# Performance work log

Hardware: AMD Instinct MI355X
Metric: run time of the kernel (lower is better)

The kernel has to match this reference:

```python
import jax, jax.numpy as jnp
import numpy as np
from jax import lax

NTIME = 2048
NCOMP = 8
HID = 64
OUT = 64
MAX_EVENTS = NTIME * NCOMP
EVENT_DIM = NCOMP + 3


def setup_inputs() -> dict:
    key = jax.random.key(0)
    ks = jax.random.split(key, 10)
    B = 64
    s = lambda fan_in: 1.0 / np.sqrt(fan_in)
    return {
        "x": jax.random.uniform(ks[0], (B, NTIME, NCOMP), dtype=jnp.float32),
        "W1": jax.random.normal(ks[1], (EVENT_DIM, HID), dtype=jnp.float32) * s(EVENT_DIM),
        "b1": jax.random.normal(ks[2], (HID,), dtype=jnp.float32) * 0.01,
        "W2": jax.random.normal(ks[3], (HID, HID), dtype=jnp.float32) * s(HID),
        "b2": jax.random.normal(ks[4], (HID,), dtype=jnp.float32) * 0.01,
        "P1": jax.random.normal(ks[5], (HID + 1, HID), dtype=jnp.float32) * s(HID + 1),
        "pb1": jax.random.normal(ks[6], (HID,), dtype=jnp.float32) * 0.01,
        "P2": jax.random.normal(ks[7], (HID, OUT), dtype=jnp.float32) * s(HID),
        "pb2": jax.random.normal(ks[8], (OUT,), dtype=jnp.float32) * 0.01,
    }


def _event_table(x):
    # x: [B, T, C] float. Vectorized run-length encoding.
    B, T, C = x.shape
    seq = jnp.transpose((x > 0.5).astype(x.dtype), (0, 2, 1))  # [B, C, T] in {0,1}
    prev = jnp.concatenate([jnp.full((B, C, 1), -1.0, x.dtype), seq[:, :, :-1]], axis=-1)
    is_start = seq != prev  # t=0 always a start; [B, C, T] bool
    t_idx = jnp.arange(T, dtype=jnp.int32)
    # position of next run start strictly after t (T if none)
    start_pos = jnp.where(is_start, t_idx, T)  # [B, C, T] int32
    shifted = jnp.concatenate([start_pos[:, :, 1:], jnp.full((B, C, 1), T, jnp.int32)], axis=-1)
    next_start = lax.cummin(shifted, axis=2, reverse=True)  # suffix min
    dur = (next_start - t_idx).astype(x.dtype)  # run length at each start slot
    max_start = max(1, T - 1)
    start_norm = (t_idx.astype(x.dtype) / max_start)  # [T]
    onehot = jnp.broadcast_to(jnp.eye(C, dtype=x.dtype)[None, :, None, :], (B, C, T, C))
    feats = jnp.stack(
        [seq, jnp.broadcast_to(start_norm, (B, C, T)), dur / T], axis=-1
    )  # [B, C, T, 3]
    rows = jnp.concatenate([onehot, feats], axis=-1)  # [B, C, T, C+3]
    mask = is_start
    rows = rows * mask[..., None].astype(x.dtype)  # masked rows zero, as in torch
    return rows.reshape(B, C * T, C + 3), mask.reshape(B, C * T)


def reference(x, W1, b1, W2, b2, P1, pb1, P2, pb2):
    rows, mask = _event_table(x)  # [B, E, 11], [B, E]
    h = jax.nn.relu(rows @ W1 + b1) @ W2 + b2  # [B, E, HID]
    h = h * mask[..., None].astype(h.dtype)
    valid = jnp.maximum(mask.sum(axis=1, keepdims=True), 1).astype(h.dtype)  # [B, 1]
    pooled = h.sum(axis=1) / valid  # [B, HID]
    z = jnp.concatenate([pooled, valid / MAX_EVENTS], axis=-1)  # [B, HID+1]
    return jax.nn.relu(z @ P1 + pb1) @ P2 + pb2  # [B, OUT]
```

## Files before the change

kernel.cpp:

```cpp
#include <hip/hip_runtime.h>
#include <hip/hip_bf16.h>

#define T_LEN 2048
#define NCOMP 8
#define HID 64
#define OUT_DIM 64
#define BATCH 64
#define MAX_EVENTS (T_LEN * NCOMP)
#define NCHUNK 32
#define PART_STRIDE 66
#define NWAVE 8

typedef unsigned long long u64;

#define PARTIAL_BYTES (64ULL * NCOMP * PART_STRIDE * 4)

__global__ __launch_bounds__(512) void event_kernel(
    const float* __restrict__ x,
    const float* __restrict__ W1,
    const float* __restrict__ b1,
    float* __restrict__ partial)
{
    const int b    = blockIdx.x & 63;
    const int c    = blockIdx.x >> 6;
    const int tid  = threadIdx.x;
    const int lane = tid & 63;
    const int wave = tid >> 6;

    __shared__ u64 wsh[NCHUNK];
    __shared__ u64 tsh[NCHUNK];
    __shared__ int nxtf[NCHUNK + 1];
    __shared__ int wtot[NWAVE];
    __shared__ float4 elist[T_LEN];
    __shared__ float Sp[NWAVE][HID];

    const float4* xp = (const float4*)(x + ((size_t)b * T_LEN) * NCOMP);
    #pragma unroll
    for (int i = 0; i < 4; ++i) {
        int t = i * 512 + tid;
        float4 v0 = xp[t * 2];
        float4 v1 = xp[t * 2 + 1];
        unsigned m = 0;
        m |= (v0.x > 0.5f) ? 1u   : 0u;
        m |= (v0.y > 0.5f) ? 2u   : 0u;
        m |= (v0.z > 0.5f) ? 4u   : 0u;
        m |= (v0.w > 0.5f) ? 8u   : 0u;
        m |= (v1.x > 0.5f) ? 16u  : 0u;
        m |= (v1.y > 0.5f) ? 32u  : 0u;
        m |= (v1.z > 0.5f) ? 64u  : 0u;
        m |= (v1.w > 0.5f) ? 128u : 0u;
        u64 wd = __ballot((m >> c) & 1u);
        if (lane == 0) wsh[i * 8 + wave] = wd;
    }
    __syncthreads();

    if (tid < NCHUNK) {
        u64 w = wsh[tid];
        u64 carry = (tid > 0) ? (wsh[tid - 1] >> 63) : 0ULL;
        u64 tr = w ^ ((w << 1) | carry);
        if (tid == 0) tr |= 1ULL;
        tsh[tid] = tr;
        int first = tr ? tid * 64 + (__ffsll((long long)tr) - 1) : T_LEN;
        #pragma unroll
        for (int off = 1; off < NCHUNK; off <<= 1) {
            int v = __shfl_down(first, off);
            if (tid + off < NCHUNK) first = (v < first) ? v : first;
        }
        nxtf[tid] = first;
        if (tid == 0) nxtf[NCHUNK] = T_LEN;
    }
    __syncthreads();

    const int ch = tid >> 4;
    const int sh = (tid & 15) * 4;
    const u64 full  = tsh[ch];
    const u64 wbits = wsh[ch];
    unsigned tr4 = (unsigned)((full >> sh) & 0xFu);
    int nt = __popc(tr4);

    int incl = nt;
    #pragma unroll
    for (int o = 1; o < 64; o <<= 1) {
        int v = __shfl_up(incl, o);
        if (lane >= o) incl += v;
    }
    if (lane == 63) wtot[wave] = incl;
    __syncthreads();
    int waveoff = 0;
    for (int w = 0; w < wave; ++w) waveoff += wtot[w];
    int nE = 0;
    #pragma unroll
    for (int w = 0; w < NWAVE; ++w) nE += wtot[w];
    int off = waveoff + incl - nt;

    unsigned rem = tr4;
    while (rem) {
        int p = __ffs(rem) - 1;
        rem &= rem - 1;
        int t = (tid << 2) + p;
        unsigned s = (unsigned)((wbits >> (sh + p)) & 1ULL);
        int nxt;
        if (rem) {
            nxt = (tid << 2) + __ffs(rem) - 1;
        } else {
            int bp = sh + 4;
            u64 above = (bp >= 64) ? 0ULL : (full & (~0ULL << bp));
            nxt = above ? ch * 64 + (__ffsll((long long)above) - 1) : nxtf[ch + 1];
        }
        elist[off].x = (float)s;
        elist[off].y = (float)t;
        elist[off].z = (float)nxt;
        elist[off].w = 0.0f;
        ++off;
    }
    __syncthreads();

    const float r8    = W1[8 * HID + lane];
    const float r9p   = W1[9 * HID + lane] * (1.0f / 2047.0f);
    const float r10p  = W1[10 * HID + lane] * (1.0f / 2048.0f);
    const float r9m   = r9p - r10p;
    const float base0 = W1[c * HID + lane] + b1[lane];

    const int oct = ((nE + 31) >> 5) << 2;
    const int i0  = wave * oct;
    const int i1  = (i0 + oct < nE) ? (i0 + oct) : nE;

    float S0 = 0.0f, S1 = 0.0f, S2 = 0.0f, S3 = 0.0f;
    int i = i0;
    for (; i + 3 < i1; i += 4) {
        float4 e0 = elist[i];
        float4 e1 = elist[i + 1];
        float4 e2 = elist[i + 2];
        float4 e3 = elist[i + 3];
        float a0 = fmaf(e0.x, r8, base0);
        float a1 = fmaf(e1.x, r8, base0);
        float a2 = fmaf(e2.x, r8, base0);
        float a3 = fmaf(e3.x, r8, base0);
        a0 = fmaf(e0.z, r10p, a0);
        a1 = fmaf(e1.z, r10p, a1);
        a2 = fmaf(e2.z, r10p, a2);
        a3 = fmaf(e3.z, r10p, a3);
        a0 = fmaf(e0.y, r9m, a0);
        a1 = fmaf(e1.y, r9m, a1);
        a2 = fmaf(e2.y, r9m, a2);
        a3 = fmaf(e3.y, r9m, a3);
        S0 += fmaxf(a0, 0.0f);
        S1 += fmaxf(a1, 0.0f);
        S2 += fmaxf(a2, 0.0f);
        S3 += fmaxf(a3, 0.0f);
    }
    for (; i < i1; ++i) {
        float4 e = elist[i];
        float a = fmaf(e.x, r8, base0);
        a = fmaf(e.z, r10p, a);
        a = fmaf(e.y, r9m, a);
        S0 += fmaxf(a, 0.0f);
    }
    Sp[wave][lane] = (S0 + S1) + (S2 + S3);
    __syncthreads();

    float* pp = partial + ((size_t)b * NCOMP + c) * PART_STRIDE;
    if (tid < HID) {
        float s = 0.0f;
        #pragma unroll
        for (int w = 0; w < NWAVE; ++w) s += Sp[w][tid];
        pp[tid] = s;
    }
    if (tid == HID) pp[HID] = (float)nE;
}

__global__ __launch_bounds__(64) void head_kernel(
    const float* __restrict__ partial,
    const float* __restrict__ W2,
    const float* __restrict__ b2,
    const float* __restrict__ P1,
    const float* __restrict__ pb1,
    const float* __restrict__ P2,
    const float* __restrict__ pb2,
    float* __restrict__ out)
{
    const int b = blockIdx.x;
    const int h = threadIdx.x;

    __shared__ float sb[HID];
    __shared__ float z[HID + 1];
    __shared__ float y[HID];

    float s = 0.0f, cnt = 0.0f;
    #pragma unroll
    for (int cc = 0; cc < NCOMP; ++cc) {
        const float* pp = partial + ((size_t)b * NCOMP + cc) * PART_STRIDE;
        s   += pp[h];
        cnt += pp[HID];
    }
    float valid = fmaxf(cnt, 1.0f);
    sb[h] = s;
    __syncthreads();

    float acc = 0.0f;
    #pragma unroll
    for (int k = 0; k < HID; ++k) acc = fmaf(sb[k], W2[k * HID + h], acc);
    z[h] = acc / valid + b2[h];
    if (h == 0) z[HID] = valid / (float)MAX_EVENTS;
    __syncthreads();

    float a1 = pb1[h];
    #pragma unroll
    for (int k = 0; k < HID + 1; ++k) a1 = fmaf(z[k], P1[k * HID + h], a1);
    y[h] = fmaxf(a1, 0.0f);
    __syncthreads();

    float o = pb2[h];
    #pragma unroll
    for (int k = 0; k < HID; ++k) o = fmaf(y[k], P2[k * HID + h], o);
    out[(size_t)b * OUT_DIM + h] = o;
}

extern "C" void kernel_launch(void* const* d_in, const int* in_sizes, int n_in,
                              void* d_out, int out_size, void* d_ws, size_t ws_size,
                              hipStream_t stream) {
    const float* x   = (const float*)d_in[0];
    const float* W1  = (const float*)d_in[1];
    const float* b1  = (const float*)d_in[2];
    const float* W2  = (const float*)d_in[3];
    const float* b2  = (const float*)d_in[4];
    const float* P1  = (const float*)d_in[5];
    const float* pb1 = (const float*)d_in[6];
    const float* P2  = (const float*)d_in[7];
    const float* pb2 = (const float*)d_in[8];
    float* out = (float*)d_out;

    float* partial = (float*)d_ws;

    event_kernel<<<BATCH * NCOMP, 512, 0, stream>>>(x, W1, b1, partial);
    head_kernel<<<BATCH, 64, 0, stream>>>(partial, W2, b2, P1, pb1, P2, pb2, out);
}
```

Baseline: 19.96 us.

## Fuse event and head kernels into one 1024-thread block per batch

Replaces the two-kernel design (512 blocks of 512 threads per batch×component, then a head kernel) with a single kernel using one 1024-thread block per batch. That block loads x once, ballots all 8 components, loops over components to build and reduce event lists, then runs the MLP head in-block. This removes a launch, the global partial buffer round trip, and the re-reading of x for every component. In exchange the grid drops to 64 blocks, which cuts parallelism on a GPU with many CUs, and the component loop serializes work behind extra barriers.

```diff
diff --git a/kernel.cpp b/kernel.cpp
--- a/kernel.cpp
+++ b/kernel.cpp
@@ -8,36 +8,41 @@
 #define BATCH 64
 #define MAX_EVENTS (T_LEN * NCOMP)
 #define NCHUNK 32
-#define PART_STRIDE 66
-#define NWAVE 8
+#define NWAVE 16
 
 typedef unsigned long long u64;
 
-#define PARTIAL_BYTES (64ULL * NCOMP * PART_STRIDE * 4)
-
-__global__ __launch_bounds__(512) void event_kernel(
+__global__ __launch_bounds__(1024) void fused_kernel(
     const float* __restrict__ x,
     const float* __restrict__ W1,
     const float* __restrict__ b1,
-    float* __restrict__ partial)
+    const float* __restrict__ W2,
+    const float* __restrict__ b2,
+    const float* __restrict__ P1,
+    const float* __restrict__ pb1,
+    const float* __restrict__ P2,
+    const float* __restrict__ pb2,
+    float* __restrict__ out)
 {
-    const int b    = blockIdx.x & 63;
-    const int c    = blockIdx.x >> 6;
+    const int b    = blockIdx.x;
     const int tid  = threadIdx.x;
     const int lane = tid & 63;
     const int wave = tid >> 6;
 
-    __shared__ u64 wsh[NCHUNK];
-    __shared__ u64 tsh[NCHUNK];
-    __shared__ int nxtf[NCHUNK + 1];
+    __shared__ u64 wsh[NCOMP][NCHUNK];
+    __shared__ u64 tsh[NCOMP][NCHUNK];
+    __shared__ int nxtf[NCOMP][NCHUNK + 1];
     __shared__ int wtot[NWAVE];
     __shared__ float4 elist[T_LEN];
     __shared__ float Sp[NWAVE][HID];
-
-    const float4* xp = (const float4*)(x + ((size_t)b * T_LEN) * NCOMP);
+    __shared__ float sb[HID];
+    __shared__ float zz[HID + 1];
+    __shared__ float yy[HID];
+
+    const float4* xp = (const float4*)(x + (size_t)b * T_LEN * NCOMP);
     #pragma unroll
-    for (int i = 0; i < 4; ++i) {
-        int t = i * 512 + tid;
+    for (int i = 0; i < 2; ++i) {
+        int t = i * 1024 + tid;
         float4 v0 = xp[t * 2];
         float4 v1 = xp[t * 2 + 1];
         unsigned m = 0;
@@ -49,69 +54,32 @@
         m |= (v1.y > 0.5f) ? 32u  : 0u;
         m |= (v1.z > 0.5f) ? 64u  : 0u;
         m |= (v1.w > 0.5f) ? 128u : 0u;
-        u64 wd = __ballot((m >> c) & 1u);
-        if (lane == 0) wsh[i * 8 + wave] = wd;
-    }
-    __syncthreads();
-
-    if (tid < NCHUNK) {
-        u64 w = wsh[tid];
-        u64 carry = (tid > 0) ? (wsh[tid - 1] >> 63) : 0ULL;
+        u64 mine = 0;
+        #pragma unroll
+        for (int c = 0; c < NCOMP; ++c) {
+            u64 wd = __ballot((m >> c) & 1u);
+            if (lane == c) mine = wd;
+        }
+        if (lane < NCOMP) wsh[lane][i * 16 + wave] = mine;
+    }
+    __syncthreads();
+
+    if (tid < NCOMP * NCHUNK) {
+        const int c = tid >> 5;
+        const int k = tid & 31;
+        u64 w = wsh[c][k];
+        u64 carry = k ? (wsh[c][k - 1] >> 63) : 0ULL;
         u64 tr = w ^ ((w << 1) | carry);
-        if (tid == 0) tr |= 1ULL;
-        tsh[tid] = tr;
-        int first = tr ? tid * 64 + (__ffsll((long long)tr) - 1) : T_LEN;
+        if (k == 0) tr |= 1ULL;
+        tsh[c][k] = tr;
+        int first = tr ? k * 64 + (__ffsll((long long)tr) - 1) : T_LEN;
         #pragma unroll
         for (int off = 1; off < NCHUNK; off <<= 1) {
             int v = __shfl_down(first, off);
-            if (tid + off < NCHUNK) first = (v < first) ? v : first;
-        }
-        nxtf[tid] = first;
-        if (tid == 0) nxtf[NCHUNK] = T_LEN;
-    }
-    __syncthreads();
-
-    const int ch = tid >> 4;
-    const int sh = (tid & 15) * 4;
-    const u64 full  = tsh[ch];
-    const u64 wbits = wsh[ch];
-    unsigned tr4 = (unsigned)((full >> sh) & 0xFu);
-    int nt = __popc(tr4);
-
-    int incl = nt;
-    #pragma unroll
-    for (int o = 1; o < 64; o <<= 1) {
-        int v = __shfl_up(incl, o);
-        if (lane >= o) incl += v;
-    }
-    if (lane == 63) wtot[wave] = incl;
-    __syncthreads();
-    int waveoff = 0;
-    for (int w = 0; w < wave; ++w) waveoff += wtot[w];
-    int nE = 0;
-    #pragma unroll
-    for (int w = 0; w < NWAVE; ++w) nE += wtot[w];
-    int off = waveoff + incl - nt;
-
-    unsigned rem = tr4;
-    while (rem) {
-        int p = __ffs(rem) - 1;
-        rem &= rem - 1;
-        int t = (tid << 2) + p;
-        unsigned s = (unsigned)((wbits >> (sh + p)) & 1ULL);
-        int nxt;
-        if (rem) {
-            nxt = (tid << 2) + __ffs(rem) - 1;
-        } else {
-            int bp = sh + 4;
-            u64 above = (bp >= 64) ? 0ULL : (full & (~0ULL << bp));
-            nxt = above ? ch * 64 + (__ffsll((long long)above) - 1) : nxtf[ch + 1];
-        }
-        elist[off].x = (float)s;
-        elist[off].y = (float)t;
-        elist[off].z = (float)nxt;
-        elist[off].w = 0.0f;
-        ++off;
+            if (k + off < NCHUNK) first = (v < first) ? v : first;
+        }
+        nxtf[c][k] = first;
+        if (k == 0) nxtf[c][NCHUNK] = T_LEN;
     }
     __syncthreads();
 
@@ -119,101 +87,151 @@
     const float r9p   = W1[9 * HID + lane] * (1.0f / 2047.0f);
     const float r10p  = W1[10 * HID + lane] * (1.0f / 2048.0f);
     const float r9m   = r9p - r10p;
-    const float base0 = W1[c * HID + lane] + b1[lane];
-
-    const int oct = ((nE + 31) >> 5) << 2;
-    const int i0  = wave * oct;
-    const int i1  = (i0 + oct < nE) ? (i0 + oct) : nE;
+    const float b1l   = b1[lane];
 
     float S0 = 0.0f, S1 = 0.0f, S2 = 0.0f, S3 = 0.0f;
-    int i = i0;
-    for (; i + 3 < i1; i += 4) {
-        float4 e0 = elist[i];
-        float4 e1 = elist[i + 1];
-        float4 e2 = elist[i + 2];
-        float4 e3 = elist[i + 3];
-        float a0 = fmaf(e0.x, r8, base0);
-        float a1 = fmaf(e1.x, r8, base0);
-        float a2 = fmaf(e2.x, r8, base0);
-        float a3 = fmaf(e3.x, r8, base0);
-        a0 = fmaf(e0.z, r10p, a0);
-        a1 = fmaf(e1.z, r10p, a1);
-        a2 = fmaf(e2.z, r10p, a2);
-        a3 = fmaf(e3.z, r10p, a3);
-        a0 = fmaf(e0.y, r9m, a0);
-        a1 = fmaf(e1.y, r9m, a1);
-        a2 = fmaf(e2.y, r9m, a2);
-        a3 = fmaf(e3.y, r9m, a3);
-        S0 += fmaxf(a0, 0.0f);
-        S1 += fmaxf(a1, 0.0f);
-        S2 += fmaxf(a2, 0.0f);
-        S3 += fmaxf(a3, 0.0f);
-    }
-    for (; i < i1; ++i) {
-        float4 e = elist[i];
-        float a = fmaf(e.x, r8, base0);
-        a = fmaf(e.z, r10p, a);
-        a = fmaf(e.y, r9m, a);
-        S0 += fmaxf(a, 0.0f);
-    }
+    int totE = 0;
+
+    for (int c = 0; c < NCOMP; ++c) {
+        int nt = 0;
+        unsigned tr4 = 0;
+        u64 full = 0, wbits = 0;
+        int ch = 0, sh = 0;
+        if (tid < 512) {
+            ch = tid >> 4;
+            sh = (tid & 15) * 4;
+            full  = tsh[c][ch];
+            wbits = wsh[c][ch];
+            tr4 = (unsigned)((full >> sh) & 0xFu);
+            nt = __popc(tr4);
+        }
+        int incl = nt;
+        #pragma unroll
+        for (int o = 1; o < 64; o <<= 1) {
+            int v = __shfl_up(incl, o);
+            if (lane >= o) incl += v;
+        }
+        if (lane == 63) wtot[wave] = incl;
+        __syncthreads();
+
+        int waveoff = 0;
+        for (int w = 0; w < wave; ++w) waveoff += wtot[w];
+        int nE = 0;
+        #pragma unroll
+        for (int w = 0; w < NWAVE; ++w) nE += wtot[w];
+        int off = waveoff + incl - nt;
+
+        unsigned rem = tr4;
+        while (rem) {
+            int p = __ffs(rem) - 1;
+            rem &= rem - 1;
+            int t = (tid << 2) + p;
+            unsigned s = (unsigned)((wbits >> (sh + p)) & 1ULL);
+            int nxt;
+            if (rem) {
+                nxt = (tid << 2) + __ffs(rem) - 1;
+            } else {
+                int bp = sh + 4;
+                u64 above = (bp >= 64) ? 0ULL : (full & (~0ULL << bp));
+                nxt = above ? ch * 64 + (__ffsll((long long)above) - 1)
+                            : nxtf[c][ch + 1];
+            }
+            float4 ev;
+            ev.x = (float)s;
+            ev.y = (float)t;
+            ev.z = (float)nxt;
+            ev.w = 0.0f;
+            elist[off++] = ev;
+        }
+        __syncthreads();
+
+        const float base0 = W1[c * HID + lane] + b1l;
+        const int span = ((nE + 63) >> 6) << 2;
+        const int i0 = wave * span;
+        const int i1 = (i0 + span < nE) ? (i0 + span) : nE;
+
+        int i = i0;
+        for (; i + 3 < i1; i += 4) {
+            float4 e0 = elist[i];
+            float4 e1 = elist[i + 1];
+            float4 e2 = elist[i + 2];
+            float4 e3 = elist[i + 3];
+            float a0 = fmaf(e0.x, r8, base0);
+            float a1 = fmaf(e1.x, r8, base0);
+            float a2 = fmaf(e2.x, r8, base0);
+            float a3 = fmaf(e3.x, r8, base0);
+            a0 = fmaf(e0.z, r10p, a0);
+            a1 = fmaf(e1.z, r10p, a1);
+            a2 = fmaf(e2.z, r10p, a2);
+            a3 = fmaf(e3.z, r10p, a3);
+            a0 = fmaf(e0.y, r9m, a0);
+            a1 = fmaf(e1.y, r9m, a1);
+            a2 = fmaf(e2.y, r9m, a2);
+            a3 = fmaf(e3.y, r9m, a3);
+            S0 += fmaxf(a0, 0.0f);
+            S1 += fmaxf(a1, 0.0f);
+            S2 += fmaxf(a2, 0.0f);
+            S3 += fmaxf(a3, 0.0f);
+        }
+        for (; i < i1; ++i) {
+            float4 e = elist[i];
+            float a = fmaf(e.x, r8, base0);
+            a = fmaf(e.z, r10p, a);
+            a = fmaf(e.y, r9m, a);
+            S0 += fmaxf(a, 0.0f);
+        }
+        totE += nE;
+    }
+
     Sp[wave][lane] = (S0 + S1) + (S2 + S3);
     __syncthreads();
 
-    float* pp = partial + ((size_t)b * NCOMP + c) * PART_STRIDE;
-    if (tid < HID) {
+    const float valid = fmaxf((float)totE, 1.0f);
+    const int h = tid;
+    if (h < HID) {
         float s = 0.0f;
         #pragma unroll
-        for (int w = 0; w < NWAVE; ++w) s += Sp[w][tid];
-        pp[tid] = s;
-    }
-    if (tid == HID) pp[HID] = (float)nE;
-}
-
-__global__ __launch_bounds__(64) void head_kernel(
-    const float* __restrict__ partial,
-    const float* __restrict__ W2,
-    const float* __restrict__ b2,
-    const float* __restrict__ P1,
-    const float* __restrict__ pb1,
-    const float* __restrict__ P2,
-    const float* __restrict__ pb2,
-    float* __restrict__ out)
-{
-    const int b = blockIdx.x;
-    const int h = threadIdx.x;
-
-    __shared__ float sb[HID];
-    __shared__ float z[HID + 1];
-    __shared__ float y[HID];
-
-    float s = 0.0f, cnt = 0.0f;
-    #pragma unroll
-    for (int cc = 0; cc < NCOMP; ++cc) {
-        const float* pp = partial + ((size_t)b * NCOMP + cc) * PART_STRIDE;
-        s   += pp[h];
-        cnt += pp[HID];
-    }
-    float valid = fmaxf(cnt, 1.0f);
-    sb[h] = s;
-    __syncthreads();
-
-    float acc = 0.0f;
-    #pragma unroll
-    for (int k = 0; k < HID; ++k) acc = fmaf(sb[k], W2[k * HID + h], acc);
-    z[h] = acc / valid + b2[h];
-    if (h == 0) z[HID] = valid / (float)MAX_EVENTS;
-    __syncthreads();
-
-    float a1 = pb1[h];
-    #pragma unroll
-    for (int k = 0; k < HID + 1; ++k) a1 = fmaf(z[k], P1[k * HID + h], a1);
-    y[h] = fmaxf(a1, 0.0f);
-    __syncthreads();
-
-    float o = pb2[h];
-    #pragma unroll
-    for (int k = 0; k < HID; ++k) o = fmaf(y[k], P2[k * HID + h], o);
-    out[(size_t)b * OUT_DIM + h] = o;
+        for (int w = 0; w < NWAVE; ++w) s += Sp[w][h];
+        sb[h] = s;
+    }
+    __syncthreads();
+    if (h < HID) {
+        float acc0 = 0.0f, acc1 = 0.0f, acc2 = 0.0f, acc3 = 0.0f;
+        #pragma unroll
+        for (int k = 0; k < HID; k += 4) {
+            acc0 = fmaf(sb[k],     W2[(k)     * HID + h], acc0);
+            acc1 = fmaf(sb[k + 1], W2[(k + 1) * HID + h], acc1);
+            acc2 = fmaf(sb[k + 2], W2[(k + 2) * HID + h], acc2);
+            acc3 = fmaf(sb[k + 3], W2[(k + 3) * HID + h], acc3);
+        }
+        zz[h] = (acc0 + acc1 + acc2 + acc3) / valid + b2[h];
+        if (h == 0) zz[HID] = valid / (float)MAX_EVENTS;
+    }
+    __syncthreads();
+    if (h < HID) {
+        float a0 = pb1[h], a1 = 0.0f, a2 = 0.0f, a3 = 0.0f;
+        #pragma unroll
+        for (int k = 0; k < HID; k += 4) {
+            a0 = fmaf(zz[k],     P1[(k)     * HID + h], a0);
+            a1 = fmaf(zz[k + 1], P1[(k + 1) * HID + h], a1);
+            a2 = fmaf(zz[k + 2], P1[(k + 2) * HID + h], a2);
+            a3 = fmaf(zz[k + 3], P1[(k + 3) * HID + h], a3);
+        }
+        a0 = fmaf(zz[HID], P1[HID * HID + h], a0);
+        yy[h] = fmaxf((a0 + a1) + (a2 + a3), 0.0f);
+    }
+    __syncthreads();
+    if (h < HID) {
+        float o0 = pb2[h], o1 = 0.0f, o2 = 0.0f, o3 = 0.0f;
+        #pragma unroll
+        for (int k = 0; k < HID; k += 4) {
+            o0 = fmaf(yy[k],     P2[(k)     * HID + h], o0);
+            o1 = fmaf(yy[k + 1], P2[(k + 1) * HID + h], o1);
+            o2 = fmaf(yy[k + 2], P2[(k + 2) * HID + h], o2);
+            o3 = fmaf(yy[k + 3], P2[(k + 3) * HID + h], o3);
+        }
+        out[(size_t)b * OUT_DIM + h] = (o0 + o1) + (o2 + o3);
+    }
 }
 
 extern "C" void kernel_launch(void* const* d_in, const int* in_sizes, int n_in,
@@ -230,8 +248,6 @@
     const float* pb2 = (const float*)d_in[8];
     float* out = (float*)d_out;
 
-    float* partial = (float*)d_ws;
-
-    event_kernel<<<BATCH * NCOMP, 512, 0, stream>>>(x, W1, b1, partial);
-    head_kernel<<<BATCH, 64, 0, stream>>>(partial, W2, b2, P1, pb1, P2, pb2, out);
+    fused_kernel<<<BATCH, 1024, 0, stream>>>(
+        x, W1, b1, W2, b2, P1, pb1, P2, pb2, out);
 }
```

Result: slower. 52.02 us (+160.7%).
